# Kernel tuning notes

Hardware: AMD Instinct MI355X
Metric: run time of the kernel (lower is better)

The kernel has to match this reference:

```python
import jax, jax.numpy as jnp
import numpy as np

IOU_THRESHOLD = 0.5


def _make_boxes(key, n, canvas=800.0, min_size=8.0, max_size=160.0):
    k1, k2 = jax.random.split(key)
    cxy = jax.random.uniform(k1, (n, 2), dtype=jnp.float32) * canvas
    wh = min_size + jax.random.uniform(k2, (n, 2), dtype=jnp.float32) * (max_size - min_size)
    return jnp.concatenate([cxy - 0.5 * wh, cxy + 0.5 * wh], axis=1)  # [n,4] x1,y1,x2,y2


def setup_inputs() -> dict:
    key = jax.random.key(0)
    kp, kg, kl = jax.random.split(key, 3)
    N, M = 262144, 256
    proposals = _make_boxes(kp, N)
    gt_boxes = _make_boxes(kg, M)
    gt_labels = jax.random.randint(kl, (M,), 1, 21, dtype=jnp.int64)  # foreground classes 1..20
    return {"proposals": proposals, "gt_boxes": gt_boxes, "gt_labels": gt_labels}


def box_iou(a, b):
    # a: [N,4], b: [M,4] in x1,y1,x2,y2 -> [N,M]
    area_a = (a[:, 2] - a[:, 0]) * (a[:, 3] - a[:, 1])
    area_b = (b[:, 2] - b[:, 0]) * (b[:, 3] - b[:, 1])
    lt = jnp.maximum(a[:, None, :2], b[None, :, :2])
    rb = jnp.minimum(a[:, None, 2:], b[None, :, 2:])
    wh = jnp.clip(rb - lt, 0.0)
    inter = wh[..., 0] * wh[..., 1]
    union = area_a[:, None] + area_b[None, :] - inter
    return inter / union


def encode_boxes(props, gts):
    pw = props[:, 2] - props[:, 0]
    ph = props[:, 3] - props[:, 1]
    px = props[:, 0] + 0.5 * pw
    py = props[:, 1] + 0.5 * ph
    gw = gts[:, 2] - gts[:, 0]
    gh = gts[:, 3] - gts[:, 1]
    gx = gts[:, 0] + 0.5 * gw
    gy = gts[:, 1] + 0.5 * gh
    tx = (gx - px) / pw
    ty = (gy - py) / ph
    tw = jnp.log(gw / pw)
    th = jnp.log(gh / ph)
    return jnp.stack([tx, ty, tw, th], axis=1)


@jax.jit
def reference(proposals, gt_boxes, gt_labels):
    iou = box_iou(proposals, gt_boxes)            # [N,M] -- the memory-bound intermediate
    max_iou = jnp.max(iou, axis=1)                # [N]
    max_idx = jnp.argmax(iou, axis=1)             # [N]
    pos_mask = max_iou >= IOU_THRESHOLD
    roi_labels = jnp.where(pos_mask, gt_labels[max_idx], jnp.zeros_like(gt_labels[max_idx]))
    matched_gt = gt_boxes[max_idx]                # [N,4]
    deltas = encode_boxes(proposals, matched_gt)  # [N,4]
    roi_reg_targets = jnp.where(pos_mask[:, None], deltas, jnp.zeros_like(deltas))
    return roi_labels, roi_reg_targets
```

## Files before the change

### kernel.cpp

```cpp
#include <hip/hip_runtime.h>

#define NGT 256

__global__ __launch_bounds__(256) void roi_assign_kernel(
    const float* __restrict__ proposals,
    const float* __restrict__ gt_boxes,
    const int*   __restrict__ gt_labels,
    float* __restrict__ out_labels,
    float* __restrict__ out_deltas,
    int N, int M)
{
    __shared__ float s_g[NGT * 4];
    __shared__ float s_area[NGT];

    for (int t = threadIdx.x; t < M * 4; t += blockDim.x) s_g[t] = gt_boxes[t];
    __syncthreads();
    for (int t = threadIdx.x; t < M; t += blockDim.x) {
        float x1 = s_g[t * 4 + 0], y1 = s_g[t * 4 + 1];
        float x2 = s_g[t * 4 + 2], y2 = s_g[t * 4 + 3];
        s_area[t] = (x2 - x1) * (y2 - y1);
    }
    __syncthreads();

    int i = blockIdx.x * blockDim.x + threadIdx.x;
    if (i >= N) return;

    float4 p = reinterpret_cast<const float4*>(proposals)[i];
    float area_a = (p.z - p.x) * (p.w - p.y);

    float best_inter = -1.0f;
    float best_union = 1.0f;
    int   best_idx   = 0;

#pragma unroll 8
    for (int j = 0; j < NGT; ++j) {
        float gx1 = s_g[j * 4 + 0], gy1 = s_g[j * 4 + 1];
        float gx2 = s_g[j * 4 + 2], gy2 = s_g[j * 4 + 3];
        float lx = fmaxf(p.x, gx1), ly = fmaxf(p.y, gy1);
        float rx = fminf(p.z, gx2), ry = fminf(p.w, gy2);
        float w = fmaxf(rx - lx, 0.0f);
        float h = fmaxf(ry - ly, 0.0f);
        float inter = w * h;
        float uni = area_a + s_area[j] - inter;
        bool upd = (inter * best_union) > (best_inter * uni);
        best_inter = upd ? inter : best_inter;
        best_union = upd ? uni   : best_union;
        best_idx   = upd ? j     : best_idx;
    }

    float max_iou = best_inter / best_union;
    bool pos = (max_iou >= 0.5f);

    int lbl = gt_labels[best_idx];
    out_labels[i] = pos ? (float)lbl : 0.0f;

    float gx1 = s_g[best_idx * 4 + 0], gy1 = s_g[best_idx * 4 + 1];
    float gx2 = s_g[best_idx * 4 + 2], gy2 = s_g[best_idx * 4 + 3];

    float pw = p.z - p.x;
    float ph = p.w - p.y;
    float px = p.x + 0.5f * pw;
    float py = p.y + 0.5f * ph;
    float gw = gx2 - gx1;
    float gh = gy2 - gy1;
    float gx = gx1 + 0.5f * gw;
    float gy = gy1 + 0.5f * gh;

    float tx = (gx - px) / pw;
    float ty = (gy - py) / ph;
    float tw = logf(gw / pw);
    float th = logf(gh / ph);

    float4 d;
    if (pos) { d.x = tx; d.y = ty; d.z = tw; d.w = th; }
    else     { d.x = 0.f; d.y = 0.f; d.z = 0.f; d.w = 0.f; }
    reinterpret_cast<float4*>(out_deltas)[i] = d;
}

extern "C" void kernel_launch(void* const* d_in, const int* in_sizes, int n_in,
                              void* d_out, int out_size, void* d_ws, size_t ws_size,
                              hipStream_t stream) {
    const float* proposals = (const float*)d_in[0];
    const float* gt_boxes  = (const float*)d_in[1];
    const int*   gt_labels = (const int*)d_in[2];

    int N = in_sizes[0] / 4;
    int M = in_sizes[1] / 4;

    float* out_labels = (float*)d_out;
    float* out_deltas = (float*)d_out + N;

    dim3 block(256);
    dim3 grid((N + 255) / 256);
    roi_assign_kernel<<<grid, block, 0, stream>>>(
        proposals, gt_boxes, gt_labels, out_labels, out_deltas, N, M);
}
```

Measured before the change: 92.47 us.

## Process two proposals per thread and read precomputed GT data via uniform loads

Adds a small prep kernel that packs each GT box with its area into a 32-byte record in workspace. The main kernel drops shared-memory staging and syncs, reading GT records from global memory with wave-uniform addresses. Each thread now handles two proposals, so every GT load is shared across two IoU evaluations. This adds a second launch and assumes N is even and M is fixed at 256.

```diff
diff --git a/kernel.cpp b/kernel.cpp
--- a/kernel.cpp
+++ b/kernel.cpp
@@ -1,70 +1,41 @@
 #include <hip/hip_runtime.h>
 
-#define NGT 256
+#define M_GT 256
 
-__global__ __launch_bounds__(256) void roi_assign_kernel(
-    const float* __restrict__ proposals,
-    const float* __restrict__ gt_boxes,
-    const int*   __restrict__ gt_labels,
-    float* __restrict__ out_labels,
-    float* __restrict__ out_deltas,
-    int N, int M)
+__global__ __launch_bounds__(256) void prep_kernel(
+    const float* __restrict__ gt_boxes, float* __restrict__ prep)
 {
-    __shared__ float s_g[NGT * 4];
-    __shared__ float s_area[NGT];
+    int j = blockIdx.x * blockDim.x + threadIdx.x;
+    if (j >= M_GT) return;
+    float x1 = gt_boxes[j * 4 + 0], y1 = gt_boxes[j * 4 + 1];
+    float x2 = gt_boxes[j * 4 + 2], y2 = gt_boxes[j * 4 + 3];
+    float area = (x2 - x1) * (y2 - y1);
+    float* o = prep + j * 8;
+    o[0] = x1; o[1] = y1; o[2] = x2; o[3] = y2;
+    o[4] = area; o[5] = 0.f; o[6] = 0.f; o[7] = 0.f;
+}
 
-    for (int t = threadIdx.x; t < M * 4; t += blockDim.x) s_g[t] = gt_boxes[t];
-    __syncthreads();
-    for (int t = threadIdx.x; t < M; t += blockDim.x) {
-        float x1 = s_g[t * 4 + 0], y1 = s_g[t * 4 + 1];
-        float x2 = s_g[t * 4 + 2], y2 = s_g[t * 4 + 3];
-        s_area[t] = (x2 - x1) * (y2 - y1);
-    }
-    __syncthreads();
-
-    int i = blockIdx.x * blockDim.x + threadIdx.x;
-    if (i >= N) return;
-
-    float4 p = reinterpret_cast<const float4*>(proposals)[i];
-    float area_a = (p.z - p.x) * (p.w - p.y);
-
-    float best_inter = -1.0f;
-    float best_union = 1.0f;
-    int   best_idx   = 0;
-
-#pragma unroll 8
-    for (int j = 0; j < NGT; ++j) {
-        float gx1 = s_g[j * 4 + 0], gy1 = s_g[j * 4 + 1];
-        float gx2 = s_g[j * 4 + 2], gy2 = s_g[j * 4 + 3];
-        float lx = fmaxf(p.x, gx1), ly = fmaxf(p.y, gy1);
-        float rx = fminf(p.z, gx2), ry = fminf(p.w, gy2);
-        float w = fmaxf(rx - lx, 0.0f);
-        float h = fmaxf(ry - ly, 0.0f);
-        float inter = w * h;
-        float uni = area_a + s_area[j] - inter;
-        bool upd = (inter * best_union) > (best_inter * uni);
-        best_inter = upd ? inter : best_inter;
-        best_union = upd ? uni   : best_union;
-        best_idx   = upd ? j     : best_idx;
-    }
-
-    float max_iou = best_inter / best_union;
+__device__ __forceinline__ void epilogue(
+    int i, float4 p, float bi, float bu, int bx,
+    const float* __restrict__ gt_boxes, const int* __restrict__ gt_labels,
+    float* __restrict__ out_labels, float* __restrict__ out_deltas)
+{
+    float max_iou = bi / bu;
     bool pos = (max_iou >= 0.5f);
 
-    int lbl = gt_labels[best_idx];
+    int lbl = gt_labels[bx];
     out_labels[i] = pos ? (float)lbl : 0.0f;
 
-    float gx1 = s_g[best_idx * 4 + 0], gy1 = s_g[best_idx * 4 + 1];
-    float gx2 = s_g[best_idx * 4 + 2], gy2 = s_g[best_idx * 4 + 3];
+    float4 g = reinterpret_cast<const float4*>(gt_boxes)[bx];
 
     float pw = p.z - p.x;
     float ph = p.w - p.y;
     float px = p.x + 0.5f * pw;
     float py = p.y + 0.5f * ph;
-    float gw = gx2 - gx1;
-    float gh = gy2 - gy1;
-    float gx = gx1 + 0.5f * gw;
-    float gy = gy1 + 0.5f * gh;
+    float gw = g.z - g.x;
+    float gh = g.w - g.y;
+    float gx = g.x + 0.5f * gw;
+    float gy = g.y + 0.5f * gh;
 
     float tx = (gx - px) / pw;
     float ty = (gy - py) / ph;
@@ -77,6 +48,65 @@
     reinterpret_cast<float4*>(out_deltas)[i] = d;
 }
 
+__global__ __launch_bounds__(256) void roi_assign_kernel(
+    const float* __restrict__ proposals,
+    const float* __restrict__ prep,
+    const float* __restrict__ gt_boxes,
+    const int*   __restrict__ gt_labels,
+    float* __restrict__ out_labels,
+    float* __restrict__ out_deltas,
+    int half)
+{
+    int t = blockIdx.x * blockDim.x + threadIdx.x;
+    if (t >= half) return;
+    int iA = t;
+    int iB = t + half;
+
+    float4 pA = reinterpret_cast<const float4*>(proposals)[iA];
+    float4 pB = reinterpret_cast<const float4*>(proposals)[iB];
+    float areaA = (pA.z - pA.x) * (pA.w - pA.y);
+    float areaB = (pB.z - pB.x) * (pB.w - pB.y);
+
+    float biA = -1.0f, buA = 1.0f; int bxA = 0;
+    float biB = -1.0f, buB = 1.0f; int bxB = 0;
+
+#pragma unroll 4
+    for (int j = 0; j < M_GT; ++j) {
+        const float4* gp = reinterpret_cast<const float4*>(prep + j * 8);
+        float4 g  = gp[0];
+        float4 g2 = gp[1];
+        float sA  = g2.x;
+
+        {
+            float lx = fmaxf(pA.x, g.x), ly = fmaxf(pA.y, g.y);
+            float rx = fminf(pA.z, g.z), ry = fminf(pA.w, g.w);
+            float w = fmaxf(rx - lx, 0.0f);
+            float h = fmaxf(ry - ly, 0.0f);
+            float inter = w * h;
+            float uni = (areaA + sA) - inter;
+            bool upd = (inter * buA) > (biA * uni);
+            biA = upd ? inter : biA;
+            buA = upd ? uni   : buA;
+            bxA = upd ? j     : bxA;
+        }
+        {
+            float lx = fmaxf(pB.x, g.x), ly = fmaxf(pB.y, g.y);
+            float rx = fminf(pB.z, g.z), ry = fminf(pB.w, g.w);
+            float w = fmaxf(rx - lx, 0.0f);
+            float h = fmaxf(ry - ly, 0.0f);
+            float inter = w * h;
+            float uni = (areaB + sA) - inter;
+            bool upd = (inter * buB) > (biB * uni);
+            biB = upd ? inter : biB;
+            buB = upd ? uni   : buB;
+            bxB = upd ? j     : bxB;
+        }
+    }
+
+    epilogue(iA, pA, biA, buA, bxA, gt_boxes, gt_labels, out_labels, out_deltas);
+    epilogue(iB, pB, biB, buB, bxB, gt_boxes, gt_labels, out_labels, out_deltas);
+}
+
 extern "C" void kernel_launch(void* const* d_in, const int* in_sizes, int n_in,
                               void* d_out, int out_size, void* d_ws, size_t ws_size,
                               hipStream_t stream) {
@@ -85,13 +115,16 @@
     const int*   gt_labels = (const int*)d_in[2];
 
     int N = in_sizes[0] / 4;
-    int M = in_sizes[1] / 4;
+    int half = N >> 1;
 
     float* out_labels = (float*)d_out;
     float* out_deltas = (float*)d_out + N;
+    float* prep = (float*)d_ws;
+
+    prep_kernel<<<1, 256, 0, stream>>>(gt_boxes, prep);
 
     dim3 block(256);
-    dim3 grid((N + 255) / 256);
+    dim3 grid((half + 255) / 256);
     roi_assign_kernel<<<grid, block, 0, stream>>>(
-        proposals, gt_boxes, gt_labels, out_labels, out_deltas, N, M);
+        proposals, prep, gt_boxes, gt_labels, out_labels, out_deltas, half);
 }
```

After: 114.8 us. +24.2%, slower.
